# Performance work log

Hardware: AMD Instinct MI355X
Metric: run time of the kernel (lower is better)

Reference implementation:

```python
import jax, jax.numpy as jnp
import numpy as np

B, L, HID, H, D = 16, 512, 768, 12, 64
NUM_STRUCT = 5


def setup_inputs() -> dict:
    key = jax.random.key(0)
    ks = jax.random.split(key, 8)
    hidden_states = jax.random.normal(ks[0], (B, L, HID), jnp.float32)
    attention_mask = jnp.zeros((B, 1, 1, L), jnp.float32)  # additive mask (0 = keep)
    structure_mask = (jax.random.uniform(ks[1], (NUM_STRUCT, B, 1, L, L)) < 0.15).astype(jnp.float32)
    s = 1.0 / np.sqrt(HID).astype(np.float32)
    Wq = jax.random.normal(ks[2], (HID, HID), jnp.float32) * s
    Wk = jax.random.normal(ks[3], (HID, HID), jnp.float32) * s
    Wv = jax.random.normal(ks[4], (HID, HID), jnp.float32) * s
    bq = jnp.zeros((HID,), jnp.float32)
    bk = jnp.zeros((HID,), jnp.float32)
    bv = jnp.zeros((HID,), jnp.float32)
    # xavier-uniform-ish scale for [D,D] biaffine mats
    xav = np.sqrt(6.0 / (D + D)).astype(np.float32)
    bili = jax.random.uniform(ks[5], (NUM_STRUCT, H, D, D), jnp.float32, -xav, xav)
    abs_bias = jnp.zeros((NUM_STRUCT, H), jnp.float32)
    return {"hidden_states": hidden_states, "attention_mask": attention_mask,
            "structure_mask": structure_mask, "Wq": Wq, "bq": bq, "Wk": Wk,
            "bk": bk, "Wv": Wv, "bv": bv, "bili": bili, "abs_bias": abs_bias}


def _heads(x, b, l):
    # [B,L,HID] -> [B,H,L,D]
    return x.reshape(b, l, H, D).transpose(0, 2, 1, 3)


def reference(hidden_states, attention_mask, structure_mask, Wq, bq, Wk, bk, Wv, bv, bili, abs_bias):
    b, l, _ = hidden_states.shape
    q = _heads(hidden_states @ Wq.T + bq, b, l)  # [B,H,L,D]
    k = _heads(hidden_states @ Wk.T + bk, b, l)
    v = _heads(hidden_states @ Wv.T + bv, b, l)

    scores = jnp.einsum('bhid,bhjd->bhij', q, k)  # [B,H,L,L]
    for i in range(NUM_STRUCT):
        bias = jnp.einsum('bhip,hpq,bhjq->bhij', q, bili[i], k)
        scores = scores + (bias + abs_bias[i][None, :, None, None]) * structure_mask[i]

    scores = scores / np.sqrt(D).astype(np.float32) + attention_mask
    probs = jax.nn.softmax(scores, axis=-1)
    ctx = jnp.einsum('bhij,bhjd->bhid', probs, v)  # [B,H,L,D]
    return ctx.transpose(0, 2, 1, 3).reshape(b, l, H * D)
```

## Files before the change

### kernel.cpp

```cpp
#include <hip/hip_runtime.h>
#include <hip/hip_bf16.h>

#define BATCH 16
#define SEQ   512
#define HID   768
#define NH    12
#define HD    64
#define NS    5
#define LOG2E 1.44269504f

typedef __attribute__((ext_vector_type(8))) short short8;
typedef __attribute__((ext_vector_type(4))) short bs4;
typedef __attribute__((ext_vector_type(4))) float floatx4;

#define MFMA16(a, b, c) __builtin_amdgcn_mfma_f32_16x16x32_bf16((a), (b), (c), 0, 0, 0)

#define GLOAD16(gp, lp) __builtin_amdgcn_global_load_lds( \
    (const __attribute__((address_space(1))) unsigned*)(gp), \
    (__attribute__((address_space(3))) unsigned*)(lp), 16, 0, 0)

static __device__ __forceinline__ short f2bs(float f) {
    unsigned x = __builtin_bit_cast(unsigned, f);
    return (short)((x + 0x7fffu + ((x >> 16) & 1u)) >> 16);
}

__global__ __launch_bounds__(256) void prep_kernel(
    const float* __restrict__ hidden, const float* __restrict__ wq,
    const float* __restrict__ wk, const float* __restrict__ wv,
    const float* __restrict__ bili, const float* __restrict__ smask,
    short* __restrict__ xb, short* __restrict__ Wb, short* __restrict__ bltb,
    unsigned char* __restrict__ mT)
{
    __shared__ short Tl[64][72];
    const int bid = blockIdx.x, tid = threadIdx.x;

    if (bid < 3072) {
        int i = bid * 256 + tid;
        float4 a = ((const float4*)hidden)[2 * i];
        float4 b = ((const float4*)hidden)[2 * i + 1];
        short8 o;
        o[0] = f2bs(a.x); o[1] = f2bs(a.y); o[2] = f2bs(a.z); o[3] = f2bs(a.w);
        o[4] = f2bs(b.x); o[5] = f2bs(b.y); o[6] = f2bs(b.z); o[7] = f2bs(b.w);
        ((short8*)xb)[i] = o;
    } else if (bid < 3936) {
        int seg = bid - 3072;
        int mat = seg / 288, blk = seg % 288;
        const float* src = (mat == 0) ? wq : (mat == 1) ? wk : wv;
        int i = blk * 256 + tid;
        float4 a = ((const float4*)src)[2 * i];
        float4 b = ((const float4*)src)[2 * i + 1];
        short8 o;
        o[0] = f2bs(a.x); o[1] = f2bs(a.y); o[2] = f2bs(a.z); o[3] = f2bs(a.w);
        o[4] = f2bs(b.x); o[5] = f2bs(b.y); o[6] = f2bs(b.z); o[7] = f2bs(b.w);
        ((short8*)(Wb + (size_t)mat * HID * HID))[i] = o;
    } else if (bid < 3996) {
        int sh = bid - 3936;
        const float* src = bili + (size_t)sh * 4096;
        short* dst = bltb + (size_t)sh * 4096;
        for (int t = tid; t < 4096; t += 256) Tl[t >> 6][t & 63] = f2bs(src[t]);
        __syncthreads();
        for (int t = tid; t < 4096; t += 256) dst[t] = Tl[t & 63][t >> 6];
    } else {
        int t = bid - 3996;
        int b = t >> 6;
        int tile = t & 63;
        int ib0 = (tile >> 3) * 64, jb0 = (tile & 7) * 64;
        unsigned char* Tb = (unsigned char*)Tl;
        const int ii = tid >> 2, jj0 = (tid & 3) * 16;
        const size_t BLL = (size_t)BATCH * SEQ * SEQ;
        const float* sm = smask + (size_t)b * SEQ * SEQ + (size_t)(ib0 + ii) * SEQ + jb0 + jj0;
        unsigned char bytes[16];
#pragma unroll
        for (int jj = 0; jj < 16; ++jj) bytes[jj] = 0;
#pragma unroll
        for (int s = 0; s < NS; ++s) {
            const float4* f = (const float4*)(sm + (size_t)s * BLL);
#pragma unroll
            for (int g = 0; g < 4; ++g) {
                float4 v = f[g];
                bytes[g * 4 + 0] |= (unsigned char)((v.x != 0.f) ? (1u << s) : 0u);
                bytes[g * 4 + 1] |= (unsigned char)((v.y != 0.f) ? (1u << s) : 0u);
                bytes[g * 4 + 2] |= (unsigned char)((v.z != 0.f) ? (1u << s) : 0u);
                bytes[g * 4 + 3] |= (unsigned char)((v.w != 0.f) ? (1u << s) : 0u);
            }
        }
#pragma unroll
        for (int jj = 0; jj < 16; ++jj) Tb[(jj0 + jj) * 80 + ii] = bytes[jj];
        __syncthreads();
        const int jT = tid >> 2, iseg = (tid & 3) * 16;
        uint4 val = *(const uint4*)&Tb[jT * 80 + iseg];
        *(uint4*)&mT[((size_t)b * SEQ + jb0 + jT) * SEQ + ib0 + iseg] = val;
    }
}

__global__ __launch_bounds__(256) void proj_mfma(
    const short* __restrict__ xb, const short* __restrict__ Wb,
    const float* __restrict__ bq, const float* __restrict__ bk, const float* __restrict__ bv,
    short* __restrict__ qo, short* __restrict__ ko, short* __restrict__ vto)
{
    __shared__ short SMEM[16384];
    short* As = SMEM;
    short* Bs = SMEM + 4096;

    const int tid = threadIdx.x, lane = tid & 63, w = tid >> 6;
    const int q4 = lane >> 4, c15 = lane & 15;
    const int m0 = blockIdx.x * 128, n0 = blockIdx.y * 128;
    const int wrow = (w & 1) * 64, wcol = (w >> 1) * 64;

    const int srow = lane >> 2;
    const int scol = (lane & 3) * 8;
    const short* gA = xb + (size_t)(m0 + w * 32 + srow) * HID + scol;
    const short* gB = Wb + (size_t)(n0 + w * 32 + srow) * HID + scol;
    short* lA = As + w * 1024;
    short* lB = Bs + w * 1024;

    floatx4 acc[4][4];
#pragma unroll
    for (int i = 0; i < 4; ++i)
#pragma unroll
        for (int j = 0; j < 4; ++j) acc[i][j] = (floatx4){0.f, 0.f, 0.f, 0.f};

    for (int k0 = 0; k0 < HID; k0 += 32) {
        __syncthreads();
        GLOAD16(gA + k0,            lA);
        GLOAD16(gA + k0 + 16 * HID, lA + 512);
        GLOAD16(gB + k0,            lB);
        GLOAD16(gB + k0 + 16 * HID, lB + 512);
        __syncthreads();

        short8 af[4], bf[4];
#pragma unroll
        for (int ri = 0; ri < 4; ++ri)
            af[ri] = *(const short8*)&As[(wrow + ri * 16 + c15) * 32 + q4 * 8];
#pragma unroll
        for (int ci = 0; ci < 4; ++ci)
            bf[ci] = *(const short8*)&Bs[(wcol + ci * 16 + c15) * 32 + q4 * 8];
#pragma unroll
        for (int ri = 0; ri < 4; ++ri)
#pragma unroll
            for (int ci = 0; ci < 4; ++ci)
                acc[ri][ci] = MFMA16(af[ri], bf[ci], acc[ri][ci]);
    }

    __syncthreads();

    short* Sw = SMEM + w * 4096;

    const int matq = n0 / HID;
    const float* bias = (matq == 0) ? bq : (matq == 1) ? bk : bv;
    const int nmBase = (n0 - matq * HID) + wcol;
    const int h = nmBase >> 6;
    const int mg0 = m0 + wrow;
    const int bb = mg0 >> 9, l0 = mg0 & 511;

    if (matq < 2) {
        const float qsc = (matq == 0) ? (0.125f * LOG2E) : 1.0f;
#pragma unroll
        for (int ci = 0; ci < 4; ++ci) {
            const int col = ci * 16 + c15;
            const float bv2 = bias[nmBase + col];
#pragma unroll
            for (int ri = 0; ri < 4; ++ri)
#pragma unroll
                for (int r = 0; r < 4; ++r) {
                    const int row = ri * 16 + q4 * 4 + r;
                    const int phys = (row << 6) + ((((col >> 3) ^ (row & 7)) << 3) | (col & 7));
                    Sw[phys] = f2bs((acc[ri][ci][r] + bv2) * qsc);
                }
        }
        short* dst = (matq == 0) ? qo : ko;
#pragma unroll
        for (int it2 = 0; it2 < 8; ++it2) {
            const int row = it2 * 8 + (lane >> 3);
            const int g = lane & 7;
            short8 val = *(const short8*)&Sw[(row << 6) + ((g ^ (row & 7)) << 3)];
            *(short8*)&dst[(((size_t)bb * NH + h) * SEQ + (l0 + row)) * HD + g * 8] = val;
        }
    } else {
#pragma unroll
        for (int ci = 0; ci < 4; ++ci) {
            const int d = ci * 16 + c15;
            const float bv2 = bias[nmBase + d];
#pragma unroll
            for (int ri = 0; ri < 4; ++ri) {
                bs4 v4;
#pragma unroll
                for (int r = 0; r < 4; ++r) v4[r] = f2bs(acc[ri][ci][r] + bv2);
                const int lbase = ri * 16 + q4 * 4;
                const int phys = (d << 6) + ((((lbase >> 3) ^ (d & 7)) << 3) | (lbase & 7));
                *(bs4*)&Sw[phys] = v4;
            }
        }
#pragma unroll
        for (int it2 = 0; it2 < 8; ++it2) {
            const int d = it2 * 8 + (lane >> 3);
            const int g = lane & 7;
            short8 val = *(const short8*)&Sw[(d << 6) + ((g ^ (d & 7)) << 3)];
            *(short8*)&vto[(((size_t)bb * NH + h) * HD + d) * SEQ + l0 + g * 8] = val;
        }
    }
}

__global__ __launch_bounds__(256) void attn_mfma(
    const short* __restrict__ q, const short* __restrict__ k, const short* __restrict__ vt,
    const unsigned char* __restrict__ mT, const float* __restrict__ amask,
    const short* __restrict__ bilit, const float* __restrict__ abs_bias,
    float* __restrict__ out)
{
    __shared__ short KsB[2][4096];
    __shared__ short VsB[2][4096];
    __shared__ short Pw[4][16 * 40];
    __shared__ float Am[SEQ];
    __shared__ float abt[32];

    const int idx = blockIdx.x;
    const int bh = idx % 192, it = idx / 192;
    const int b = bh / NH, h = bh % NH;
    const int i0 = it * 64;
    const int tid = threadIdx.x, lane = tid & 63, w = tid >> 6;
    const int q4 = lane >> 4, c15 = lane & 15, x7 = c15 & 7;

    const short* qg = q + (size_t)bh * SEQ * HD;
    const short* kg = k + (size_t)bh * SEQ * HD;
    const short* vg = vt + (size_t)bh * HD * SEQ;

    const int s0 = w * 128 + lane;
    const int r0 = s0 >> 3, cg0 = (s0 & 7) ^ (r0 & 7);
    const int s1 = s0 + 64;
    const int r1 = s1 >> 3, cg1 = (s1 & 7) ^ (r1 & 7);

    GLOAD16(kg + (size_t)r0 * HD + cg0 * 8, &KsB[0][w * 1024]);
    GLOAD16(kg + (size_t)r1 * HD + cg1 * 8, &KsB[0][w * 1024 + 512]);
    GLOAD16(vg + (size_t)r0 * SEQ + cg0 * 8, &VsB[0][w * 1024]);
    GLOAD16(vg + (size_t)r1 * SEQ + cg1 * 8, &VsB[0][w * 1024 + 512]);

    if (tid < 32) {
        float a = 0.f;
#pragma unroll
        for (int s = 0; s < NS; ++s)
            if (tid & (1u << s)) a += abs_bias[s * NH + h];
        abt[tid] = a * (0.125f * LOG2E) - 23.0f;
    }
    for (int c = tid; c < SEQ; c += 256) Am[c] = amask[b * SEQ + c] * LOG2E;

    short8 aQ0 = *(const short8*)&qg[(size_t)(i0 + w * 16 + c15) * HD + q4 * 8];
    short8 aQ1 = *(const short8*)&qg[(size_t)(i0 + w * 16 + c15) * HD + 32 + q4 * 8];

    short* pw = &Pw[w][0];
    short8 aP[NS][2];
#pragma unroll
    for (int s = 0; s < NS; ++s) {
        const short* bt = bilit + ((size_t)s * NH + h) * 4096;
#pragma unroll
        for (int half = 0; half < 2; ++half) {
#pragma unroll
            for (int n2 = 0; n2 < 2; ++n2) {
                const int ns = half * 2 + n2;
                short8 bf0 = *(const short8*)&bt[(ns * 16 + c15) * 64 + q4 * 8];
                short8 bf1 = *(const short8*)&bt[(ns * 16 + c15) * 64 + 32 + q4 * 8];
                floatx4 acc = {0.f, 0.f, 0.f, 0.f};
                acc = MFMA16(aQ0, bf0, acc);
                acc = MFMA16(aQ1, bf1, acc);
#pragma unroll
                for (int r = 0; r < 4; ++r)
                    pw[(q4 * 4 + r) * 40 + n2 * 16 + c15] = f2bs(acc[r]);
            }
            aP[s][half] = *(const short8*)&pw[c15 * 40 + q4 * 8];
        }
    }

    float l_part[4] = {0.f, 0.f, 0.f, 0.f};
    floatx4 O[4];
#pragma unroll
    for (int d = 0; d < 4; ++d) O[d] = (floatx4){0.f, 0.f, 0.f, 0.f};

    const int ibase = i0 + w * 16 + q4 * 4;
    const unsigned char* mTb = mT + (size_t)b * SEQ * SEQ;

    unsigned mv[4];
#pragma unroll
    for (int js = 0; js < 4; ++js)
        mv[js] = *(const unsigned*)&mTb[(size_t)(js * 16 + c15) * SEQ + ibase];

    for (int jt = 0; jt < 8; ++jt) {
        const int j0 = jt * 64;
        __syncthreads();

        unsigned mvn[4] = {0u, 0u, 0u, 0u};
        if (jt < 7) {
            const int jn = j0 + 64;
            short* kb_ = &KsB[(jt + 1) & 1][w * 1024];
            short* vb_ = &VsB[(jt + 1) & 1][w * 1024];
            GLOAD16(kg + (size_t)(jn + r0) * HD + cg0 * 8, kb_);
            GLOAD16(kg + (size_t)(jn + r1) * HD + cg1 * 8, kb_ + 512);
            GLOAD16(vg + (size_t)r0 * SEQ + jn + cg0 * 8, vb_);
            GLOAD16(vg + (size_t)r1 * SEQ + jn + cg1 * 8, vb_ + 512);
#pragma unroll
            for (int js = 0; js < 4; ++js)
                mvn[js] = *(const unsigned*)&mTb[(size_t)(jn + js * 16 + c15) * SEQ + ibase];
        }

        const short* Kc = KsB[jt & 1];
        const short* Vc = VsB[jt & 1];

#pragma unroll
        for (int js = 0; js < 4; ++js) {
            const int row = js * 16 + c15;
            short8 kf0 = *(const short8*)&Kc[row * 64 + ((q4 ^ x7) << 3)];
            short8 kf1 = *(const short8*)&Kc[row * 64 + (((4 + q4) ^ x7) << 3)];

            floatx4 a0 = {0.f, 0.f, 0.f, 0.f};
            a0 = MFMA16(aQ0, kf0, a0);
            a0 = MFMA16(aQ1, kf1, a0);
            floatx4 as_[NS];
#pragma unroll
            for (int s = 0; s < NS; ++s) {
                floatx4 tacc = {0.f, 0.f, 0.f, 0.f};
                tacc = MFMA16(aP[s][0], kf0, tacc);
                tacc = MFMA16(aP[s][1], kf1, tacc);
                as_[s] = tacc;
            }
            const float amv = Am[j0 + js * 16 + c15];
#pragma unroll
            for (int r = 0; r < 4; ++r) {
                const unsigned mbyte = (mv[js] >> (8 * r)) & 0xffu;
                float sc = a0[r] + amv + abt[mbyte & 31u];
#pragma unroll
                for (int s = 0; s < NS; ++s)
                    sc = fmaf((float)((mbyte >> s) & 1u), as_[s][r], sc);
                float p = __builtin_amdgcn_exp2f(sc);
                l_part[r] += p;
                pw[(q4 * 4 + r) * 40 + (js & 1) * 16 + c15] = f2bs(p);
            }
            if (js & 1) {
                short8 pA = *(const short8*)&pw[c15 * 40 + q4 * 8];
                const int kk = js >> 1;
#pragma unroll
                for (int d = 0; d < 4; ++d) {
                    const int vrow = d * 16 + c15;
                    short8 vb = *(const short8*)&Vc[vrow * 64 + (((kk * 4 + q4) ^ x7) << 3)];
                    O[d] = MFMA16(pA, vb, O[d]);
                }
            }
        }
#pragma unroll
        for (int js = 0; js < 4; ++js) mv[js] = mvn[js];
    }

#pragma unroll
    for (int r = 0; r < 4; ++r) {
        float l = l_part[r];
        l += __shfl_xor(l, 1);
        l += __shfl_xor(l, 2);
        l += __shfl_xor(l, 4);
        l += __shfl_xor(l, 8);
        float inv = 1.f / l;
        float* orow = out + ((size_t)b * SEQ + ibase + r) * HID + h * HD;
#pragma unroll
        for (int d = 0; d < 4; ++d)
            orow[d * 16 + c15] = O[d][r] * inv;
    }
}

extern "C" void kernel_launch(void* const* d_in, const int* in_sizes, int n_in,
                              void* d_out, int out_size, void* d_ws, size_t ws_size,
                              hipStream_t stream) {
    const float* hidden   = (const float*)d_in[0];
    const float* amask    = (const float*)d_in[1];
    const float* smask    = (const float*)d_in[2];
    const float* Wq       = (const float*)d_in[3];
    const float* bq       = (const float*)d_in[4];
    const float* Wk       = (const float*)d_in[5];
    const float* bk       = (const float*)d_in[6];
    const float* Wv       = (const float*)d_in[7];
    const float* bv       = (const float*)d_in[8];
    const float* bili     = (const float*)d_in[9];
    const float* abs_bias = (const float*)d_in[10];
    float* out = (float*)d_out;

    char* ws = (char*)d_ws;
    const size_t QKV = (size_t)BATCH * NH * SEQ * HD * 2;
    short* qb   = (short*)(ws);
    short* kb   = (short*)(ws + QKV);
    short* vtb  = (short*)(ws + 2 * QKV);
    short* xb   = (short*)(ws + 3 * QKV);
    short* Wb   = (short*)(ws + 4 * QKV);
    short* bltb = (short*)(ws + 4 * QKV + (size_t)3 * HID * HID * 2);
    unsigned char* mT = (unsigned char*)(ws + 4 * QKV + (size_t)3 * HID * HID * 2
                                         + (size_t)NS * NH * HD * HD * 2);

    prep_kernel<<<5020, 256, 0, stream>>>(hidden, Wq, Wk, Wv, bili, smask,
                                          xb, Wb, bltb, mT);

    proj_mfma<<<dim3(BATCH * SEQ / 128, 3 * HID / 128), 256, 0, stream>>>(
        xb, Wb, bq, bk, bv, qb, kb, vtb);

    attn_mfma<<<(SEQ / 64) * NH * BATCH, 256, 0, stream>>>(
        qb, kb, vtb, mT, amask, bltb, abs_bias, out);
}
```

Before: 321.9 us.

## Double-buffer projection GEMM LDS loads and repack structure mask as dwords

The QKV projection GEMM now uses two LDS buffers. The global-to-LDS loads for the next K slice are issued before the MFMAs on the current slice, which removes one barrier per iteration and overlaps load latency with compute. The mask-packing prologue now has each thread read a 4x4 block of the five structure masks and assemble packed bytes into dwords. It stores whole dwords into the LDS transpose tile instead of 16 single-byte writes. The double buffer doubles the LDS used by the GEMM main loop, and the prefetch relies on the barrier draining the previous loads.

```diff
diff --git a/kernel.cpp b/kernel.cpp
--- a/kernel.cpp
+++ b/kernel.cpp
@@ -65,31 +65,31 @@
         int b = t >> 6;
         int tile = t & 63;
         int ib0 = (tile >> 3) * 64, jb0 = (tile & 7) * 64;
-        unsigned char* Tb = (unsigned char*)Tl;
-        const int ii = tid >> 2, jj0 = (tid & 3) * 16;
+        unsigned* Ml = (unsigned*)Tl;
         const size_t BLL = (size_t)BATCH * SEQ * SEQ;
-        const float* sm = smask + (size_t)b * SEQ * SEQ + (size_t)(ib0 + ii) * SEQ + jb0 + jj0;
-        unsigned char bytes[16];
-#pragma unroll
-        for (int jj = 0; jj < 16; ++jj) bytes[jj] = 0;
+        const int rg = tid >> 4, cg = tid & 15;
+        const float* sm = smask + ((size_t)b * SEQ + (ib0 + 4 * rg)) * SEQ + jb0 + 4 * cg;
+        unsigned dw[4] = {0u, 0u, 0u, 0u};
 #pragma unroll
         for (int s = 0; s < NS; ++s) {
-            const float4* f = (const float4*)(sm + (size_t)s * BLL);
-#pragma unroll
-            for (int g = 0; g < 4; ++g) {
-                float4 v = f[g];
-                bytes[g * 4 + 0] |= (unsigned char)((v.x != 0.f) ? (1u << s) : 0u);
-                bytes[g * 4 + 1] |= (unsigned char)((v.y != 0.f) ? (1u << s) : 0u);
-                bytes[g * 4 + 2] |= (unsigned char)((v.z != 0.f) ? (1u << s) : 0u);
-                bytes[g * 4 + 3] |= (unsigned char)((v.w != 0.f) ? (1u << s) : 0u);
-            }
-        }
-#pragma unroll
-        for (int jj = 0; jj < 16; ++jj) Tb[(jj0 + jj) * 80 + ii] = bytes[jj];
+            const float* ss = sm + (size_t)s * BLL;
+#pragma unroll
+            for (int rr = 0; rr < 4; ++rr) {
+                float4 v = *(const float4*)(ss + (size_t)rr * SEQ);
+                const unsigned bit = (1u << s);
+                dw[0] |= (v.x != 0.f) ? (bit << (8 * rr)) : 0u;
+                dw[1] |= (v.y != 0.f) ? (bit << (8 * rr)) : 0u;
+                dw[2] |= (v.z != 0.f) ? (bit << (8 * rr)) : 0u;
+                dw[3] |= (v.w != 0.f) ? (bit << (8 * rr)) : 0u;
+            }
+        }
+#pragma unroll
+        for (int cc = 0; cc < 4; ++cc)
+            Ml[(4 * cg + cc) * 20 + rg] = dw[cc];
         __syncthreads();
-        const int jT = tid >> 2, iseg = (tid & 3) * 16;
-        uint4 val = *(const uint4*)&Tb[jT * 80 + iseg];
-        *(uint4*)&mT[((size_t)b * SEQ + jb0 + jT) * SEQ + ib0 + iseg] = val;
+        const int j = tid >> 2, ig = tid & 3;
+        uint4 val = *(const uint4*)&Ml[j * 20 + 4 * ig];
+        *(uint4*)&mT[((size_t)b * SEQ + jb0 + j) * SEQ + ib0 + 16 * ig] = val;
     }
 }
 
@@ -99,8 +99,6 @@
     short* __restrict__ qo, short* __restrict__ ko, short* __restrict__ vto)
 {
     __shared__ short SMEM[16384];
-    short* As = SMEM;
-    short* Bs = SMEM + 4096;
 
     const int tid = threadIdx.x, lane = tid & 63, w = tid >> 6;
     const int q4 = lane >> 4, c15 = lane & 15;
@@ -111,8 +109,6 @@
     const int scol = (lane & 3) * 8;
     const short* gA = xb + (size_t)(m0 + w * 32 + srow) * HID + scol;
     const short* gB = Wb + (size_t)(n0 + w * 32 + srow) * HID + scol;
-    short* lA = As + w * 1024;
-    short* lB = Bs + w * 1024;
 
     floatx4 acc[4][4];
 #pragma unroll
@@ -120,13 +116,29 @@
 #pragma unroll
         for (int j = 0; j < 4; ++j) acc[i][j] = (floatx4){0.f, 0.f, 0.f, 0.f};
 
-    for (int k0 = 0; k0 < HID; k0 += 32) {
+    {
+        short* lA = SMEM + w * 1024;
+        short* lB = SMEM + 4096 + w * 1024;
+        GLOAD16(gA,            lA);
+        GLOAD16(gA + 16 * HID, lA + 512);
+        GLOAD16(gB,            lB);
+        GLOAD16(gB + 16 * HID, lB + 512);
+    }
+
+    for (int it = 0; it < HID / 32; ++it) {
         __syncthreads();
-        GLOAD16(gA + k0,            lA);
-        GLOAD16(gA + k0 + 16 * HID, lA + 512);
-        GLOAD16(gB + k0,            lB);
-        GLOAD16(gB + k0 + 16 * HID, lB + 512);
-        __syncthreads();
+        if (it + 1 < HID / 32) {
+            const int k0 = (it + 1) * 32;
+            short* base = SMEM + ((it + 1) & 1) * 8192;
+            short* lA = base + w * 1024;
+            short* lB = base + 4096 + w * 1024;
+            GLOAD16(gA + k0,            lA);
+            GLOAD16(gA + k0 + 16 * HID, lA + 512);
+            GLOAD16(gB + k0,            lB);
+            GLOAD16(gB + k0 + 16 * HID, lB + 512);
+        }
+        const short* As = SMEM + (it & 1) * 8192;
+        const short* Bs = As + 4096;
 
         short8 af[4], bf[4];
 #pragma unroll
```

Measured after the change: 308.9 us. 4.0% less time.
